# Optimization experiments

Measured on AMD Instinct MI355X. Metric: run time of the kernel, lower is better.

Reference implementation:

```python
import jax, jax.numpy as jnp
import numpy as np

EPS = 1e-05
DECAY = 0.99
K = 2048   # codebook_size
D = 256    # codebook_dim


def setup_inputs() -> dict:
    key = jax.random.key(0)
    k1, k2, k3 = jax.random.split(key, 3)
    hidden_states = jax.random.normal(k1, (16, 4096, D), dtype=jnp.float32)
    embed_sum = jax.random.normal(k2, (K, D), dtype=jnp.float32)
    cluster_usage = jax.random.uniform(k3, (K,), dtype=jnp.float32)
    return {"hidden_states": hidden_states, "embed_sum": embed_sum, "cluster_usage": cluster_usage}


def reference(hidden_states, embed_sum, cluster_usage):
    # embed property: embed_sum / clamp(cluster_usage, min=eps)
    embed = embed_sum / jnp.clip(cluster_usage, EPS, None)[:, None]  # [K, D]

    shape = hidden_states.shape
    flat = hidden_states.reshape(-1, shape[-1])  # [N, D]

    # quantize: cdist(p=2) + argmin. argmin over squared distances is identical
    # to argmin over euclidean distances, avoiding the sqrt.
    x2 = jnp.sum(flat * flat, axis=-1, keepdims=True)          # [N, 1]
    e2 = jnp.sum(embed * embed, axis=-1)[None, :]              # [1, K]
    d2 = x2 - 2.0 * (flat @ embed.T) + e2                      # [N, K]
    flat_ind = jnp.argmin(d2, axis=-1)                         # [N]

    embed_ind = flat_ind.reshape(shape[:-1])                   # [B, T]
    quantize = embed[flat_ind].reshape(shape)                  # [B, T, D]

    # training-path EMA accumulation (scatter_add -> segment_sum), functional form
    counts = jax.ops.segment_sum(jnp.ones_like(flat_ind, dtype=flat.dtype), flat_ind, num_segments=K)
    sums = jax.ops.segment_sum(flat, flat_ind, num_segments=K)  # [K, D]
    new_cluster_usage = cluster_usage * DECAY + counts * (1.0 - DECAY)
    new_embed_sum = embed_sum * DECAY + sums * (1.0 - DECAY)

    return quantize, embed_ind, new_cluster_usage, new_embed_sum
```

## Files before the change

### kernel.cpp

```cpp
#include <hip/hip_runtime.h>

#define EPSF 1e-5f
#define DECAYF 0.99f
#define KCODES 2048
#define DIM 256
#define CC 64

typedef _Float16 f16;
typedef f16 f16x8 __attribute__((ext_vector_type(8)));
typedef float f32x4 __attribute__((ext_vector_type(4)));

#define MFMA16(A, B, C) __builtin_amdgcn_mfma_f32_16x16x32_f16(A, B, C, 0, 0, 0)

#define OFF_AH 0
#define OFF_AL 16384
#define OFF_BH 32768
#define OFF_BL 49152

__device__ __forceinline__ void gload_lds16(const void* g, void* l) {
    __builtin_amdgcn_global_load_lds(
        (const __attribute__((address_space(1))) void*)g,
        (__attribute__((address_space(3))) void*)l, 16, 0, 0);
}

__global__ __launch_bounds__(256) void split_x_kernel(
    const float* __restrict__ x, f16* __restrict__ xh, f16* __restrict__ xl, int n8)
{
    int i = blockIdx.x * 256 + threadIdx.x;
    if (i >= n8) return;
    f32x4 v0 = ((const f32x4*)x)[2 * i];
    f32x4 v1 = ((const f32x4*)x)[2 * i + 1];
    f16x8 h, l;
    #pragma unroll
    for (int t = 0; t < 4; ++t) {
        f16 h0 = (f16)v0[t]; h[t] = h0; l[t] = (f16)(v0[t] - (float)h0);
        f16 h1 = (f16)v1[t]; h[t + 4] = h1; l[t + 4] = (f16)(v1[t] - (float)h1);
    }
    ((f16x8*)xh)[i] = h;
    ((f16x8*)xl)[i] = l;
}

__global__ __launch_bounds__(256) void prep_embed_kernel(
    const float* __restrict__ embed_sum, const float* __restrict__ usage,
    float* __restrict__ embed, f16* __restrict__ eh, f16* __restrict__ el,
    float* __restrict__ e2)
{
    int k = blockIdx.x;
    int d = threadIdx.x;
    float inv = 1.0f / fmaxf(usage[k], EPSF);
    float e = embed_sum[k * DIM + d] * inv;
    embed[k * DIM + d] = e;
    float ec = fminf(fmaxf(e, -65000.0f), 65000.0f);
    f16 h = (f16)ec;
    f16 l = (f16)(ec - (float)h);
    eh[k * DIM + d] = h;
    el[k * DIM + d] = l;
    float sq = e * e;
    #pragma unroll
    for (int off = 32; off > 0; off >>= 1) sq += __shfl_down(sq, off, 64);
    __shared__ float ws[4];
    if ((threadIdx.x & 63) == 0) ws[threadIdx.x >> 6] = sq;
    __syncthreads();
    if (threadIdx.x == 0) e2[k] = ws[0] + ws[1] + ws[2] + ws[3];
}

__global__ __launch_bounds__(512, 2) void argmin_kernel(
    const f16* __restrict__ xh, const f16* __restrict__ xl,
    const f16* __restrict__ eh, const f16* __restrict__ el,
    const float* __restrict__ e2, int* __restrict__ flat_ind, int* __restrict__ cnt)
{
    __shared__ __align__(1024) char lds[2 * 65536 + 8192];
    float* e2s = (float*)(lds + 131072);

    const int tid  = threadIdx.x;
    const int w    = tid >> 6, lane = tid & 63;
    const int l15  = lane & 15, l4 = lane >> 4;
    const int wm   = w >> 1, wn = w & 1;
    const int row0 = blockIdx.x * 256;
    const int gsw  = (lane & 3) ^ ((lane >> 3) & 3);
    const int lq   = lane >> 2;
    const int rslot = (l4 ^ ((l15 >> 1) & 3)) * 16;

    f32x4 acc[4][8];
    f16x8 a[4], b[8];
    float best[16];
    int   bidx[16];
    #pragma unroll
    for (int t = 0; t < 16; ++t) { best[t] = 3.4e38f; bidx[t] = 0; }

    auto stageU = [&](const f16* rowbase, int koff, char* unit) {
        #pragma unroll
        for (int q = 0; q < 2; ++q) {
            const int r = w * 32 + q * 16 + lq;
            gload_lds16(rowbase + (size_t)r * DIM + koff + gsw * 8,
                        unit + w * 2048 + q * 1024 + lane * 16);
        }
    };
    auto readA = [&](const char* unit) {
        #pragma unroll
        for (int i = 0; i < 4; ++i)
            a[i] = *(const f16x8*)(unit + (wm * 64 + i * 16 + l15) * 64 + rslot);
    };
    auto readB = [&](const char* unit) {
        #pragma unroll
        for (int j = 0; j < 8; ++j)
            b[j] = *(const f16x8*)(unit + (wn * 128 + j * 16 + l15) * 64 + rslot);
    };
    auto mf = [&]() {
        #pragma unroll
        for (int i = 0; i < 4; ++i)
            #pragma unroll
            for (int j = 0; j < 8; ++j)
                acc[i][j] = MFMA16(a[i], b[j], acc[i][j]);
    };

    ((f32x4*)e2s)[tid] = ((const f32x4*)e2)[tid];
    asm volatile("s_waitcnt vmcnt(0)" ::: "memory");
    stageU(xh + (size_t)row0 * DIM, 0, lds + OFF_AH);
    stageU(eh, 0, lds + OFF_BH);
    stageU(el, 0, lds + OFF_BL);
    stageU(xl + (size_t)row0 * DIM, 0, lds + OFF_AL);

    for (int cc = 0; cc < CC; ++cc) {
        char* buf  = lds + (cc & 1) * 65536;
        char* nbuf = lds + ((cc + 1) & 1) * 65536;
        const int ct = cc >> 3, sd = cc & 7;
        const int nct = (cc + 1) >> 3, nsd = (cc + 1) & 7;
        const bool more = (cc + 1 < CC);

        if (sd == 0) {
            #pragma unroll
            for (int i = 0; i < 4; ++i)
                #pragma unroll
                for (int j = 0; j < 8; ++j)
                    acc[i][j] = (f32x4){0.f, 0.f, 0.f, 0.f};
        }

        if (more) {
            stageU(xh + (size_t)row0 * DIM, nsd * 32, nbuf + OFF_AH);
            stageU(eh + (size_t)(nct * 256) * DIM, nsd * 32, nbuf + OFF_BH);
            asm volatile("s_waitcnt vmcnt(8)" ::: "memory");
        } else {
            asm volatile("s_waitcnt vmcnt(4)" ::: "memory");
        }
        __builtin_amdgcn_s_barrier();
        __builtin_amdgcn_sched_barrier(0);
        readA(buf + OFF_AH);
        readB(buf + OFF_BH);
        __builtin_amdgcn_s_setprio(1);
        mf();
        __builtin_amdgcn_s_setprio(0);
        __builtin_amdgcn_s_barrier();

        if (more) {
            stageU(el + (size_t)(nct * 256) * DIM, nsd * 32, nbuf + OFF_BL);
            asm volatile("s_waitcnt vmcnt(8)" ::: "memory");
        } else {
            asm volatile("s_waitcnt vmcnt(2)" ::: "memory");
        }
        __builtin_amdgcn_s_barrier();
        __builtin_amdgcn_sched_barrier(0);
        readB(buf + OFF_BL);
        __builtin_amdgcn_s_setprio(1);
        mf();
        __builtin_amdgcn_s_setprio(0);
        __builtin_amdgcn_s_barrier();

        if (more) {
            stageU(xl + (size_t)row0 * DIM, nsd * 32, nbuf + OFF_AL);
            asm volatile("s_waitcnt vmcnt(8)" ::: "memory");
        } else {
            asm volatile("s_waitcnt vmcnt(0)" ::: "memory");
        }
        __builtin_amdgcn_s_barrier();
        __builtin_amdgcn_sched_barrier(0);
        readA(buf + OFF_AL);
        readB(buf + OFF_BH);
        __builtin_amdgcn_s_setprio(1);
        mf();
        __builtin_amdgcn_s_setprio(0);
        __builtin_amdgcn_s_barrier();

        if (sd == 7) {
            const int cbase = ct * 256 + wn * 128;
            #pragma unroll
            for (int j = 0; j < 8; ++j) {
                const int col = cbase + j * 16 + l15;
                const float e2v = e2s[col];
                #pragma unroll
                for (int i = 0; i < 4; ++i)
                    #pragma unroll
                    for (int r = 0; r < 4; ++r) {
                        float m = fmaf(-2.0f, acc[i][j][r], e2v);
                        const int tt_ = i * 4 + r;
                        if (m < best[tt_]) { best[tt_] = m; bidx[tt_] = col; }
                    }
            }
        }
    }

    __syncthreads();
    float* rv = (float*)lds;
    int*   ri = (int*)(lds + 4096);
    #pragma unroll
    for (int tt_ = 0; tt_ < 16; ++tt_) {
        float v = best[tt_];
        int  ix = bidx[tt_];
        #pragma unroll
        for (int m = 1; m <= 8; m <<= 1) {
            float ov = __shfl_xor(v, m, 64);
            int  oix = __shfl_xor(ix, m, 64);
            if (ov < v || (ov == v && oix < ix)) { v = ov; ix = oix; }
        }
        if (l15 == 0) {
            const int rl = wm * 64 + (tt_ >> 2) * 16 + l4 * 4 + (tt_ & 3);
            rv[rl * 2 + wn] = v;
            ri[rl * 2 + wn] = ix;
        }
    }
    __syncthreads();
    if (tid < 256) {
        float v0 = rv[tid * 2], v1 = rv[tid * 2 + 1];
        int   i0 = ri[tid * 2], i1 = ri[tid * 2 + 1];
        int ib = (v1 < v0 || (v1 == v0 && i1 < i0)) ? i1 : i0;
        flat_ind[row0 + tid] = ib;
        unsigned long long pending = ~0ULL;
        while (pending) {
            int leader = __ffsll((long long)pending) - 1;
            int lind = __shfl(ib, leader, 64);
            unsigned long long same = __ballot(ib == lind);
            if ((tid & 63) == leader) atomicAdd(&cnt[lind], (int)__popcll(same));
            pending &= ~same;
        }
    }
}

__global__ __launch_bounds__(256) void scan_kernel(
    const int* __restrict__ cnt, int* __restrict__ offs, int* __restrict__ cursor)
{
    __shared__ int ps[256];
    const int t = threadIdx.x;
    int pre[8], s = 0;
    #pragma unroll
    for (int j = 0; j < 8; ++j) { pre[j] = s; s += cnt[t * 8 + j]; }
    ps[t] = s;
    __syncthreads();
    for (int off = 1; off < 256; off <<= 1) {
        int v = (t >= off) ? ps[t - off] : 0;
        __syncthreads();
        ps[t] += v;
        __syncthreads();
    }
    int ex = (t > 0) ? ps[t - 1] : 0;
    #pragma unroll
    for (int j = 0; j < 8; ++j) {
        offs[t * 8 + j]   = ex + pre[j];
        cursor[t * 8 + j] = ex + pre[j];
    }
}

__global__ __launch_bounds__(256) void assign_kernel(
    const int* __restrict__ flat_ind, int* __restrict__ cursor,
    int* __restrict__ rowlist, int* __restrict__ codesorted)
{
    const int i    = blockIdx.x * 256 + threadIdx.x;
    const int lane = threadIdx.x & 63;
    const int ind  = flat_ind[i];
    int pos = 0;
    unsigned long long pending = ~0ULL;
    while (pending) {
        int leader = __ffsll((long long)pending) - 1;
        int lind = __shfl(ind, leader, 64);
        unsigned long long same = __ballot(ind == lind);
        if (ind == lind) {
            int base = 0;
            if (lane == leader) base = atomicAdd(&cursor[lind], (int)__popcll(same));
            base = __shfl(base, leader, 64);
            pos = base + (int)__popcll(same & ((1ULL << lane) - 1ULL));
        }
        pending &= ~same;
    }
    rowlist[pos] = i;
    codesorted[pos] = ind;
}

__global__ __launch_bounds__(256) void codesum_kernel(
    const float* __restrict__ x, const int* __restrict__ rowlist,
    const int* __restrict__ codesorted, float* __restrict__ sums)
{
    const int p0 = blockIdx.x * 64;
    __shared__ int rows[64], codes[64];
    if (threadIdx.x < 64) {
        rows[threadIdx.x]  = rowlist[p0 + threadIdx.x];
        codes[threadIdx.x] = codesorted[p0 + threadIdx.x];
    }
    __syncthreads();
    const int d = threadIdx.x;
    float acc = 0.f;
    int cur = codes[0];
    #pragma unroll 4
    for (int r = 0; r < 64; ++r) {
        const int c = codes[r];
        if (c != cur) {
            atomicAdd(&sums[(size_t)cur * DIM + d], acc);
            acc = 0.f; cur = c;
        }
        acc += x[(size_t)rows[r] * DIM + d];
    }
    atomicAdd(&sums[(size_t)cur * DIM + d], acc);
}

__global__ __launch_bounds__(256) void finalize_kernel(
    const float* __restrict__ embed_sum, const float* __restrict__ usage,
    const float* __restrict__ sums, const int* __restrict__ cnt,
    float* __restrict__ out_usage, float* __restrict__ out_es)
{
    const int k = blockIdx.x, d = threadIdx.x;
    out_es[k * DIM + d] = embed_sum[k * DIM + d] * DECAYF + sums[k * DIM + d] * (1.0f - DECAYF);
    if (d == 0)
        out_usage[k] = usage[k] * DECAYF + (float)cnt[k] * (1.0f - DECAYF);
}

__global__ __launch_bounds__(256) void quantize_kernel(
    const float* __restrict__ embed, const int* __restrict__ flat_ind,
    float* __restrict__ out_q, float* __restrict__ out_ind_f, int N)
{
    int i = blockIdx.x * 256 + threadIdx.x;
    int row = i >> 6, c4 = i & 63;
    int ind = flat_ind[row];
    ((f32x4*)out_q)[i] = ((const f32x4*)embed)[ind * 64 + c4];
    if (i < N) out_ind_f[i] = (float)flat_ind[i];
}

extern "C" void kernel_launch(void* const* d_in, const int* in_sizes, int n_in,
                              void* d_out, int out_size, void* d_ws, size_t ws_size,
                              hipStream_t stream)
{
    const float* hs        = (const float*)d_in[0];
    const float* embed_sum = (const float*)d_in[1];
    const float* usage     = (const float*)d_in[2];
    const int N = in_sizes[0] / DIM;

    float* ws_f      = (float*)d_ws;
    float* embed     = ws_f;
    float* e2        = embed + KCODES * DIM;
    float* sums      = e2 + KCODES;
    f16*   eh        = (f16*)(sums + KCODES * DIM);
    f16*   el        = eh + KCODES * DIM;
    int*   cnt       = (int*)(el + KCODES * DIM);
    int*   offs      = cnt + KCODES;
    int*   cursor    = offs + KCODES;
    int*   rowlist   = cursor + KCODES;
    int*   codesorted= rowlist + N;
    int*   flat_ind  = codesorted + N;

    float* out_q     = (float*)d_out;
    float* out_ind   = out_q + (size_t)N * DIM;
    float* out_usage = out_ind + N;
    float* out_es    = out_usage + KCODES;

    f16* xh = (f16*)out_q;
    f16* xl = xh + (size_t)N * DIM;

    hipMemsetAsync(cnt, 0, KCODES * sizeof(int), stream);
    hipMemsetAsync(sums, 0, (size_t)KCODES * DIM * sizeof(float), stream);

    split_x_kernel<<<(N * DIM / 8 + 255) / 256, 256, 0, stream>>>(hs, xh, xl, N * DIM / 8);
    prep_embed_kernel<<<KCODES, 256, 0, stream>>>(embed_sum, usage, embed, eh, el, e2);
    argmin_kernel<<<N / 256, 512, 0, stream>>>(xh, xl, eh, el, e2, flat_ind, cnt);
    scan_kernel<<<1, 256, 0, stream>>>(cnt, offs, cursor);
    assign_kernel<<<N / 256, 256, 0, stream>>>(flat_ind, cursor, rowlist, codesorted);
    codesum_kernel<<<N / 64, 256, 0, stream>>>(hs, rowlist, codesorted, sums);
    finalize_kernel<<<KCODES, 256, 0, stream>>>(embed_sum, usage, sums, cnt, out_usage, out_es);
    quantize_kernel<<<N * DIM / 4 / 256, 256, 0, stream>>>(embed, flat_ind, out_q, out_ind, N);
}
```

Before: 300.7 us.

## Collapse three-phase split-f16 MFMA pipeline into single-barrier stage per chunk

Replaces the three sub-phases per K-chunk, each with its own partial vmcnt wait and barrier pair, with one full wait and one barrier per chunk. All four next-chunk tiles are then issued at once, and the hi/lo operand fragments are read together so the three MFMA passes run back to back. This is meant to cut barrier and synchronisation overhead, at the cost of higher register pressure from keeping more fragments live. Overlap of loads with compute also becomes coarser, since the wait for every outstanding load now happens before the barrier at the top of each chunk.

```diff
diff --git a/kernel.cpp b/kernel.cpp
--- a/kernel.cpp
+++ b/kernel.cpp
@@ -82,7 +82,6 @@
     const int rslot = (l4 ^ ((l15 >> 1) & 3)) * 16;
 
     f32x4 acc[4][8];
-    f16x8 a[4], b[8];
     float best[16];
     int   bidx[16];
     #pragma unroll
@@ -96,37 +95,20 @@
                         unit + w * 2048 + q * 1024 + lane * 16);
         }
     };
-    auto readA = [&](const char* unit) {
-        #pragma unroll
-        for (int i = 0; i < 4; ++i)
-            a[i] = *(const f16x8*)(unit + (wm * 64 + i * 16 + l15) * 64 + rslot);
-    };
-    auto readB = [&](const char* unit) {
-        #pragma unroll
-        for (int j = 0; j < 8; ++j)
-            b[j] = *(const f16x8*)(unit + (wn * 128 + j * 16 + l15) * 64 + rslot);
-    };
-    auto mf = [&]() {
-        #pragma unroll
-        for (int i = 0; i < 4; ++i)
-            #pragma unroll
-            for (int j = 0; j < 8; ++j)
-                acc[i][j] = MFMA16(a[i], b[j], acc[i][j]);
-    };
 
     ((f32x4*)e2s)[tid] = ((const f32x4*)e2)[tid];
-    asm volatile("s_waitcnt vmcnt(0)" ::: "memory");
     stageU(xh + (size_t)row0 * DIM, 0, lds + OFF_AH);
+    stageU(xl + (size_t)row0 * DIM, 0, lds + OFF_AL);
     stageU(eh, 0, lds + OFF_BH);
     stageU(el, 0, lds + OFF_BL);
-    stageU(xl + (size_t)row0 * DIM, 0, lds + OFF_AL);
 
     for (int cc = 0; cc < CC; ++cc) {
         char* buf  = lds + (cc & 1) * 65536;
         char* nbuf = lds + ((cc + 1) & 1) * 65536;
         const int ct = cc >> 3, sd = cc & 7;
-        const int nct = (cc + 1) >> 3, nsd = (cc + 1) & 7;
-        const bool more = (cc + 1 < CC);
+        const int nn = cc + 1;
+        const int nct = nn >> 3, nsd = nn & 7;
+        const bool more = (nn < CC);
 
         if (sd == 0) {
             #pragma unroll
@@ -136,50 +118,47 @@
                     acc[i][j] = (f32x4){0.f, 0.f, 0.f, 0.f};
         }
 
+        asm volatile("s_waitcnt vmcnt(0)" ::: "memory");
+        __builtin_amdgcn_s_barrier();
+        __builtin_amdgcn_sched_barrier(0);
+
         if (more) {
             stageU(xh + (size_t)row0 * DIM, nsd * 32, nbuf + OFF_AH);
+            stageU(xl + (size_t)row0 * DIM, nsd * 32, nbuf + OFF_AL);
             stageU(eh + (size_t)(nct * 256) * DIM, nsd * 32, nbuf + OFF_BH);
-            asm volatile("s_waitcnt vmcnt(8)" ::: "memory");
-        } else {
-            asm volatile("s_waitcnt vmcnt(4)" ::: "memory");
-        }
-        __builtin_amdgcn_s_barrier();
-        __builtin_amdgcn_sched_barrier(0);
-        readA(buf + OFF_AH);
-        readB(buf + OFF_BH);
-        __builtin_amdgcn_s_setprio(1);
-        mf();
-        __builtin_amdgcn_s_setprio(0);
-        __builtin_amdgcn_s_barrier();
-
-        if (more) {
             stageU(el + (size_t)(nct * 256) * DIM, nsd * 32, nbuf + OFF_BL);
-            asm volatile("s_waitcnt vmcnt(8)" ::: "memory");
-        } else {
-            asm volatile("s_waitcnt vmcnt(2)" ::: "memory");
-        }
-        __builtin_amdgcn_s_barrier();
-        __builtin_amdgcn_sched_barrier(0);
-        readB(buf + OFF_BL);
-        __builtin_amdgcn_s_setprio(1);
-        mf();
-        __builtin_amdgcn_s_setprio(0);
-        __builtin_amdgcn_s_barrier();
-
-        if (more) {
-            stageU(xl + (size_t)row0 * DIM, nsd * 32, nbuf + OFF_AL);
-            asm volatile("s_waitcnt vmcnt(8)" ::: "memory");
-        } else {
-            asm volatile("s_waitcnt vmcnt(0)" ::: "memory");
-        }
-        __builtin_amdgcn_s_barrier();
-        __builtin_amdgcn_sched_barrier(0);
-        readA(buf + OFF_AL);
-        readB(buf + OFF_BH);
-        __builtin_amdgcn_s_setprio(1);
-        mf();
-        __builtin_amdgcn_s_setprio(0);
-        __builtin_amdgcn_s_barrier();
+        }
+
+        f16x8 ah[4], al[4], bh[8], bl[8];
+        #pragma unroll
+        for (int i = 0; i < 4; ++i)
+            ah[i] = *(const f16x8*)(buf + OFF_AH + (wm * 64 + i * 16 + l15) * 64 + rslot);
+        #pragma unroll
+        for (int j = 0; j < 8; ++j)
+            bh[j] = *(const f16x8*)(buf + OFF_BH + (wn * 128 + j * 16 + l15) * 64 + rslot);
+        #pragma unroll
+        for (int i = 0; i < 4; ++i)
+            al[i] = *(const f16x8*)(buf + OFF_AL + (wm * 64 + i * 16 + l15) * 64 + rslot);
+
+        #pragma unroll
+        for (int i = 0; i < 4; ++i)
+            #pragma unroll
+            for (int j = 0; j < 8; ++j)
+                acc[i][j] = MFMA16(ah[i], bh[j], acc[i][j]);
+        #pragma unroll
+        for (int i = 0; i < 4; ++i)
+            #pragma unroll
+            for (int j = 0; j < 8; ++j)
+                acc[i][j] = MFMA16(al[i], bh[j], acc[i][j]);
+
+        #pragma unroll
+        for (int j = 0; j < 8; ++j)
+            bl[j] = *(const f16x8*)(buf + OFF_BL + (wn * 128 + j * 16 + l15) * 64 + rslot);
+        #pragma unroll
+        for (int i = 0; i < 4; ++i)
+            #pragma unroll
+            for (int j = 0; j < 8; ++j)
+                acc[i][j] = MFMA16(ah[i], bl[j], acc[i][j]);
 
         if (sd == 7) {
             const int cbase = ct * 256 + wn * 128;
```

Measured after the change: 289.0 us. 1.04x faster.
